# Kernel tuning notes

Measured on AMD Instinct MI355X. Metric: run time of the kernel, lower is better.

## Reference

```python
import jax, jax.numpy as jnp
import numpy as np

SOS_INDEX = 1  # args.sos_index
EOS_INDEX = 2  # args.eos_index

V, H, T, B = 32000, 1024, 32, 64


def setup_inputs() -> dict:
    key = jax.random.key(0)
    ks = jax.random.split(key, 10)
    s = 0.05  # weight scale to keep softmax/tanh in a sane range
    return {
        "E": jax.random.normal(ks[0], (V, H), jnp.float32) * s,          # embedding table
        "W_ih": jax.random.normal(ks[1], (4 * H, H), jnp.float32) * s,   # LSTMCell input weights (i,f,g,o)
        "W_hh": jax.random.normal(ks[2], (4 * H, H), jnp.float32) * s,
        "b_ih": jax.random.normal(ks[3], (4 * H,), jnp.float32) * s,
        "b_hh": jax.random.normal(ks[4], (4 * H,), jnp.float32) * s,
        "W_out": jax.random.normal(ks[5], (V, H), jnp.float32) * s,      # self.out Linear
        "b_out": jnp.zeros((V,), jnp.float32),
        "encoder_hidden": jax.random.normal(ks[6], (B, H), jnp.float32),
        "encoder_cell": jax.random.normal(ks[7], (B, H), jnp.float32),
        "target_var": jax.random.randint(ks[8], (T, B), 0, V),
        "target_max_len": T,
    }


def reference(E, W_ih, W_hh, b_ih, b_hh, W_out, b_out,
              encoder_hidden, encoder_cell, target_var, target_max_len):
    # Eval-mode decode: use_teacher_forcing = False -> greedy argmax feedback.
    batch = encoder_hidden.shape[0]
    x0 = E[jnp.full((batch,), SOS_INDEX)]  # embedding(SOS) for every batch element

    def step(carry, _):
        x, h, c = carry
        # PyTorch LSTMCell: gates ordered (i, f, g, o)
        gates = x @ W_ih.T + b_ih + h @ W_hh.T + b_hh      # [B, 4H]
        i, f, g, o = jnp.split(gates, 4, axis=1)
        c_new = jax.nn.sigmoid(f) * c + jax.nn.sigmoid(i) * jnp.tanh(g)
        h_new = jax.nn.sigmoid(o) * jnp.tanh(c_new)
        logits = h_new @ W_out.T + b_out                    # [B, V]
        mask = jax.nn.softmax(logits, axis=1)[:, EOS_INDEX] # [B]
        # greedy feedback: topk(1) == argmax
        x_next = E[jnp.argmax(logits, axis=1)]              # [B, H]
        return (x_next, h_new, c_new), (logits, mask)

    _, (outputs, masks) = jax.lax.scan(
        step, (x0, encoder_hidden, encoder_cell), None, length=target_max_len)
    return outputs, masks  # [T, B, V], [T, B]
```

## Files before the change

kernel.cpp:

```cpp
#include <hip/hip_runtime.h>
#include <math.h>


typedef short bf16x8 __attribute__((ext_vector_type(8)));
typedef unsigned short ush8 __attribute__((ext_vector_type(8)));
typedef float f32x4 __attribute__((ext_vector_type(4)));

constexpr int kH = 1024;
constexpr int kFH = 4096;
constexpr int kB = 64;
constexpr int kV = 32000;
constexpr int kT = 32;
constexpr int kSOS = 1;
constexpr int kEOS = 2;

__device__ inline unsigned short f2bf(float f) {
  unsigned int u = __float_as_uint(f);
  u += 0x7fffu + ((u >> 16) & 1u);
  return (unsigned short)(u >> 16);
}
__device__ inline float bf2f(unsigned short h) {
  return __uint_as_float(((unsigned int)h) << 16);
}

__global__ __launch_bounds__(256) void init_kernel(
    const float* __restrict__ eh, const float* __restrict__ ec,
    float* __restrict__ ws) {
  int g = blockIdx.x * 256 + threadIdx.x;
  float* h = ws + 65536;
  float* c = ws + 131072;
  if (g < 65536) {
    int u = g >> 6, b = g & 63;
    c[u * 64 + b] = ec[(size_t)b * kH + u];
  } else {
    int i = g - 65536;
    int u = i >> 6, b = i & 63;
    h[i] = eh[(size_t)b * kH + u];
  }
}

__global__ __launch_bounds__(256) void wsplit_kernel(
    const float* __restrict__ W, unsigned short* __restrict__ hi,
    unsigned short* __restrict__ lo) {
  size_t i = ((size_t)blockIdx.x * 256 + threadIdx.x) * 4;
  float4 w = *(const float4*)(W + i);
  unsigned short h0 = f2bf(w.x), h1 = f2bf(w.y), h2 = f2bf(w.z), h3 = f2bf(w.w);
  ushort4 hv = make_ushort4(h0, h1, h2, h3);
  ushort4 lv = make_ushort4(f2bf(w.x - bf2f(h0)), f2bf(w.y - bf2f(h1)),
                            f2bf(w.z - bf2f(h2)), f2bf(w.w - bf2f(h3)));
  *(ushort4*)(hi + i) = hv;
  *(ushort4*)(lo + i) = lv;
}

__global__ __launch_bounds__(256) void gates_kernel(
    const float* __restrict__ Wih, const float* __restrict__ Whh,
    const float* __restrict__ E, const float* __restrict__ h,
    float* __restrict__ part, const float* __restrict__ pmax_g,
    const float* __restrict__ psum_g, const int* __restrict__ pidx_g,
    const float* __restrict__ out_prev, float* __restrict__ mask_prev, int t) {
  __shared__ __align__(16) float Wt[64 * 68];
  __shared__ __align__(16) float Zt[64 * 68];
  __shared__ const float* rowp[64];
  __shared__ float redA[4][64];
  __shared__ int redI[4][64];
  __shared__ float redS[4][64];
  const int tid = threadIdx.x;
  const int s = blockIdx.y;
  const int r0 = blockIdx.x * 64;
  const int phase = s >> 2;
  const int kc0 = (s & 3) * 256;
  const float* __restrict__ W = phase ? Whh : Wih;

  if (!phase) {
    const int b = tid & 63, kq = tid >> 6;
    if (t == 0) {
      if (tid < 64) rowp[tid] = E + (size_t)kSOS * kH;
    } else {
      float mx = -INFINITY;
      int ix = 0x7fffffff;
      for (int k = kq; k < 250; k += 4) {
        float v = pmax_g[k * 64 + b];
        int ii = pidx_g[k * 64 + b];
        if (v > mx || (v == mx && ii < ix)) { mx = v; ix = ii; }
      }
      redA[kq][b] = mx;
      redI[kq][b] = ix;
      __syncthreads();
      if (tid < 64) {
        float M = redA[0][tid];
        int ai = redI[0][tid];
#pragma unroll
        for (int w2 = 1; w2 < 4; ++w2) {
          float v = redA[w2][tid];
          int ii = redI[w2][tid];
          if (v > M || (v == M && ii < ai)) { M = v; ai = ii; }
        }
        rowp[tid] = E + (size_t)ai * kH;
        redA[0][tid] = M;
      }
      if (blockIdx.x == 0) {
        __syncthreads();
        float M = redA[0][b];
        float sacc = 0.f;
        for (int k = kq; k < 250; k += 4)
          sacc += psum_g[k * 64 + b] * expf(pmax_g[k * 64 + b] - M);
        redS[kq][b] = sacc;
        __syncthreads();
        if (tid < 64) {
          float S = redS[0][tid] + redS[1][tid] + redS[2][tid] + redS[3][tid];
          mask_prev[tid] = expf(out_prev[(size_t)tid * kV + kEOS] - M) / S;
        }
      }
    }
  }
  __syncthreads();

  const int tb4 = tid & 15;
  const int tr4 = tid >> 4;
  float acc[4][4];
#pragma unroll
  for (int i = 0; i < 4; ++i)
#pragma unroll
    for (int j = 0; j < 4; ++j) acc[i][j] = 0.f;

  for (int kc = kc0; kc < kc0 + 256; kc += 64) {
#pragma unroll
    for (int l = 0; l < 4; ++l) {
      int f4 = tid + 256 * l;
      int row = f4 >> 4;
      int c4 = f4 & 15;
      float4 w = *(const float4*)(W + (size_t)(r0 + row) * kH + kc + c4 * 4);
      float wv[4] = {w.x, w.y, w.z, w.w};
#pragma unroll
      for (int cc = 0; cc < 4; ++cc) {
        int c = (cc + c4) & 3;
        Wt[(c4 * 4 + c) * 68 + row] = wv[c];
      }
    }
    if (!phase) {
#pragma unroll
      for (int l = 0; l < 4; ++l) {
        int g = tid + 256 * l;
        int zb = g >> 4, k4 = g & 15;
        f32x4 v = *(const f32x4*)(rowp[zb] + kc + k4 * 4);
#pragma unroll
        for (int j = 0; j < 4; ++j) Zt[(k4 * 4 + j) * 68 + zb] = v[j];
      }
    } else {
#pragma unroll
      for (int l = 0; l < 4; ++l) {
        int f4 = tid + 256 * l;
        int kk = f4 >> 4;
        int b4 = f4 & 15;
        *(float4*)(&Zt[kk * 68 + b4 * 4]) =
            *(const float4*)(h + (size_t)(kc + kk) * 64 + b4 * 4);
      }
    }
    __syncthreads();
#pragma unroll
    for (int kk = 0; kk < 64; ++kk) {
      float4 a = *(const float4*)(&Wt[kk * 68 + tr4 * 4]);
      float4 zb = *(const float4*)(&Zt[kk * 68 + tb4 * 4]);
      float av[4] = {a.x, a.y, a.z, a.w};
      float zv[4] = {zb.x, zb.y, zb.z, zb.w};
#pragma unroll
      for (int i = 0; i < 4; ++i)
#pragma unroll
        for (int j = 0; j < 4; ++j) acc[i][j] += av[i] * zv[j];
    }
    __syncthreads();
  }
#pragma unroll
  for (int i = 0; i < 4; ++i) {
    float4 o = make_float4(acc[i][0], acc[i][1], acc[i][2], acc[i][3]);
    *(float4*)(&part[((size_t)s * kFH + r0 + tr4 * 4 + i) * 64 + tb4 * 4]) = o;
  }
}

__global__ __launch_bounds__(256) void lstm_kernel(
    const float* __restrict__ part, const float* __restrict__ bih,
    const float* __restrict__ bhh, float* __restrict__ h,
    float* __restrict__ c, unsigned short* __restrict__ Hhi,
    unsigned short* __restrict__ Hlo) {
  int g = blockIdx.x * 256 + threadIdx.x;
  int b = g & 63, u = g >> 6;
  float gate[4];
#pragma unroll
  for (int ty = 0; ty < 4; ++ty) {
    int r = ty * kH + u;
    float acc = bih[r] + bhh[r];
#pragma unroll
    for (int s2 = 0; s2 < 8; ++s2)
      acc += part[((size_t)s2 * kFH + r) * 64 + b];
    gate[ty] = acc;
  }
  float gi = 1.f / (1.f + expf(-gate[0]));
  float gf = 1.f / (1.f + expf(-gate[1]));
  float gg = tanhf(gate[2]);
  float go = 1.f / (1.f + expf(-gate[3]));
  float cn = gf * c[g] + gi * gg;
  float hn = go * tanhf(cn);
  c[g] = cn;
  h[g] = hn;
  unsigned short hb = f2bf(hn);
  Hhi[(size_t)b * kH + u] = hb;
  Hlo[(size_t)b * kH + u] = f2bf(hn - bf2f(hb));
}

__global__ __launch_bounds__(256) void logits_mfma_kernel(
    const unsigned short* __restrict__ Whi, const unsigned short* __restrict__ Wlo,
    const unsigned short* __restrict__ Hhi, const unsigned short* __restrict__ Hlo,
    const float* __restrict__ bout, float* __restrict__ out,
    float* __restrict__ pmax_g, float* __restrict__ psum_g,
    int* __restrict__ pidx_g) {
  __shared__ __align__(16) unsigned short Hs[8192];
  const int tid = threadIdx.x;
  const int wave = tid >> 6, lane = tid & 63;
  const int m = lane & 15, q = lane >> 4;
  const int v0 = blockIdx.x * 128 + wave * 32;
  const unsigned short* wp0 = Whi + (size_t)(v0 + m) * kH + q * 8;
  const unsigned short* wp1 = Whi + (size_t)(v0 + 16 + m) * kH + q * 8;
  const unsigned short* lp0 = Wlo + (size_t)(v0 + m) * kH + q * 8;
  const unsigned short* lp1 = Wlo + (size_t)(v0 + 16 + m) * kH + q * 8;

  const unsigned short* sptr[4];
  int sdst[4];
#pragma unroll
  for (int l = 0; l < 4; ++l) {
    int g = tid + 256 * l;
    int tile = g >> 9, row = (g >> 3) & 63, cg = g & 7;
    sptr[l] = (tile ? Hlo : Hhi) + (size_t)row * kH + cg * 8;
    sdst[l] = tile * 4096 + row * 64 + ((cg ^ (row & 7)) * 8);
  }

  f32x4 acc[2][4];
#pragma unroll
  for (int tv = 0; tv < 2; ++tv)
#pragma unroll
    for (int bt = 0; bt < 4; ++bt) acc[tv][bt] = (f32x4){0.f, 0.f, 0.f, 0.f};

  struct WF { bf16x8 ah[2], al[2]; };
  WF w0, w1;
  ush8 hreg[4];

  auto loadW = [&](WF& f, int ko) {
    f.ah[0] = *(const bf16x8*)(wp0 + ko);
    f.ah[1] = *(const bf16x8*)(wp1 + ko);
    f.al[0] = *(const bf16x8*)(lp0 + ko);
    f.al[1] = *(const bf16x8*)(lp1 + ko);
  };
  auto loadH = [&](int kc) {
#pragma unroll
    for (int l = 0; l < 4; ++l) hreg[l] = *(const ush8*)(sptr[l] + kc);
  };
  auto readHfrag = [&](bf16x8 bh[4], bf16x8 bl[4], int koff) {
    int gbase = q + (koff >> 3);
#pragma unroll
    for (int bt = 0; bt < 4; ++bt) {
      int row = bt * 16 + m;
      int off = row * 64 + ((gbase ^ (row & 7)) * 8);
      bh[bt] = *(const bf16x8*)(Hs + off);
      bl[bt] = *(const bf16x8*)(Hs + 4096 + off);
    }
  };
  auto mfma3 = [&](const WF& f, bf16x8 bh[4], bf16x8 bl[4]) {
#pragma unroll
    for (int tv = 0; tv < 2; ++tv)
#pragma unroll
      for (int bt = 0; bt < 4; ++bt) {
        acc[tv][bt] = __builtin_amdgcn_mfma_f32_16x16x32_bf16(
            f.ah[tv], bh[bt], acc[tv][bt], 0, 0, 0);
        acc[tv][bt] = __builtin_amdgcn_mfma_f32_16x16x32_bf16(
            f.ah[tv], bl[bt], acc[tv][bt], 0, 0, 0);
        acc[tv][bt] = __builtin_amdgcn_mfma_f32_16x16x32_bf16(
            f.al[tv], bh[bt], acc[tv][bt], 0, 0, 0);
      }
  };

  loadH(0);
  loadW(w0, 0);
  for (int kc = 0; kc < kH; kc += 64) {
    __syncthreads();
#pragma unroll
    for (int l = 0; l < 4; ++l) *(ush8*)(Hs + sdst[l]) = hreg[l];
    __syncthreads();
    if (kc + 64 < kH) loadH(kc + 64);
    bf16x8 bh[4], bl[4];
    loadW(w1, kc + 32);
    readHfrag(bh, bl, 0);
    mfma3(w0, bh, bl);
    if (kc + 64 < kH) loadW(w0, kc + 64);
    readHfrag(bh, bl, 32);
    mfma3(w1, bh, bl);
  }

  float4 bo0 = *(const float4*)(bout + v0 + q * 4);
  float4 bo1 = *(const float4*)(bout + v0 + 16 + q * 4);
#pragma unroll
  for (int tv = 0; tv < 2; ++tv) {
    float4 bo = tv ? bo1 : bo0;
#pragma unroll
    for (int bt = 0; bt < 4; ++bt) {
      int b = bt * 16 + m;
      f32x4 a = acc[tv][bt];
      a[0] += bo.x; a[1] += bo.y; a[2] += bo.z; a[3] += bo.w;
      acc[tv][bt] = a;
      float4 o = make_float4(a[0], a[1], a[2], a[3]);
      *(float4*)(out + (size_t)b * kV + v0 + tv * 16 + q * 4) = o;
    }
  }

  __shared__ float lred[4][4][64];
  __shared__ int lidx[4][4][64];
  __shared__ float bbm[64];
  const int blk = blockIdx.x;
  const int vbase = blk * 128;

#pragma unroll
  for (int bt = 0; bt < 4; ++bt) {
    float pmv = -INFINITY;
    int piv = 0x7fffffff;
#pragma unroll
    for (int tv = 0; tv < 2; ++tv)
#pragma unroll
      for (int r = 0; r < 4; ++r) {
        float val = acc[tv][bt][r];
        int v = vbase + wave * 32 + tv * 16 + q * 4 + r;
        if (val > pmv) { pmv = val; piv = v; }
      }
    lred[wave][q][bt * 16 + m] = pmv;
    lidx[wave][q][bt * 16 + m] = piv;
  }
  __syncthreads();
  if (tid < 64) {
    float bm = -INFINITY;
    int bi = 0x7fffffff;
#pragma unroll
    for (int w = 0; w < 4; ++w)
#pragma unroll
      for (int qq = 0; qq < 4; ++qq) {
        float v2 = lred[w][qq][tid];
        int i2 = lidx[w][qq][tid];
        if (v2 > bm || (v2 == bm && i2 < bi)) { bm = v2; bi = i2; }
      }
    bbm[tid] = bm;
    pmax_g[(size_t)blk * 64 + tid] = bm;
    pidx_g[(size_t)blk * 64 + tid] = bi;
  }
  __syncthreads();
#pragma unroll
  for (int bt = 0; bt < 4; ++bt) {
    float bm = bbm[bt * 16 + m];
    float s = 0.f;
#pragma unroll
    for (int tv = 0; tv < 2; ++tv)
#pragma unroll
      for (int r = 0; r < 4; ++r) s += expf(acc[tv][bt][r] - bm);
    lred[wave][q][bt * 16 + m] = s;
  }
  __syncthreads();
  if (tid < 64) {
    float s = 0.f;
#pragma unroll
    for (int w = 0; w < 4; ++w)
#pragma unroll
      for (int qq = 0; qq < 4; ++qq) s += lred[w][qq][tid];
    psum_g[(size_t)blk * 64 + tid] = s;
  }
}

__global__ __launch_bounds__(256) void final_mask_kernel(
    const float* __restrict__ pm, const float* __restrict__ ps,
    const float* __restrict__ out_t, float* __restrict__ mask) {
  __shared__ float rm[4][64];
  __shared__ float rs[4][64];
  const int tid = threadIdx.x;
  const int b = tid & 63, kq = tid >> 6;
  float mx = -INFINITY;
  for (int k = kq; k < 250; k += 4) {
    float v = pm[k * 64 + b];
    if (v > mx) mx = v;
  }
  rm[kq][b] = mx;
  __syncthreads();
  if (tid < 64) {
    float M = fmaxf(fmaxf(rm[0][tid], rm[1][tid]), fmaxf(rm[2][tid], rm[3][tid]));
    rm[0][tid] = M;
  }
  __syncthreads();
  float M = rm[0][b];
  float s = 0.f;
  for (int k = kq; k < 250; k += 4)
    s += ps[k * 64 + b] * expf(pm[k * 64 + b] - M);
  rs[kq][b] = s;
  __syncthreads();
  if (tid < 64) {
    float S = rs[0][tid] + rs[1][tid] + rs[2][tid] + rs[3][tid];
    mask[tid] = expf(out_t[(size_t)tid * kV + kEOS] - M) / S;
  }
}

extern "C" void kernel_launch(void* const* d_in, const int* in_sizes, int n_in,
                              void* d_out, int out_size, void* d_ws,
                              size_t ws_size, hipStream_t stream) {
  const float* E = (const float*)d_in[0];
  const float* Wih = (const float*)d_in[1];
  const float* Whh = (const float*)d_in[2];
  const float* bih = (const float*)d_in[3];
  const float* bhh = (const float*)d_in[4];
  const float* Wout = (const float*)d_in[5];
  const float* bout = (const float*)d_in[6];
  const float* eh = (const float*)d_in[7];
  const float* ec = (const float*)d_in[8];
  float* out = (float*)d_out;
  float* ws = (float*)d_ws;

  float* h = ws + 65536;
  float* c = ws + 131072;
  float* part = ws + 196608;
  float* pmaxg = ws + 2293760;
  float* psumg = ws + 2310144;
  int* pidxg = (int*)(ws + 2326528);
  unsigned short* Whi = (unsigned short*)(ws + 2359296);
  unsigned short* Wlo = Whi + (size_t)kV * kH;
  unsigned short* Hhi = Wlo + (size_t)kV * kH;
  unsigned short* Hlo = Hhi + (size_t)kB * kH;
  float* maskbase = out + (size_t)kT * kB * kV;

  init_kernel<<<512, 256, 0, stream>>>(eh, ec, ws);
  wsplit_kernel<<<kV, 256, 0, stream>>>(Wout, Whi, Wlo);
  for (int t = 0; t < kT; ++t) {
    float* out_t = out + (size_t)t * kB * kV;
    const float* out_prev = t ? out + (size_t)(t - 1) * kB * kV : nullptr;
    float* mask_prev = t ? maskbase + (size_t)(t - 1) * kB : nullptr;
    gates_kernel<<<dim3(64, 8), 256, 0, stream>>>(
        Wih, Whh, E, h, part, pmaxg, psumg, pidxg, out_prev, mask_prev, t);
    lstm_kernel<<<256, 256, 0, stream>>>(part, bih, bhh, h, c, Hhi, Hlo);
    logits_mfma_kernel<<<250, 256, 0, stream>>>(Whi, Wlo, Hhi, Hlo, bout,
                                                out_t, pmaxg, psumg, pidxg);
  }
  final_mask_kernel<<<1, 256, 0, stream>>>(
      pmaxg, psumg, out + (size_t)(kT - 1) * kB * kV,
      maskbase + (size_t)(kT - 1) * kB);
}
```

Before: 3.390 ms.

## Halve logits tile per block and stream H from global with 3-stage register prefetch

The logits kernel now gives each block 64 vocab rows instead of 128, so it launches 500 blocks instead of 250 and fills more of the GPU's compute units. The shared-memory staging of H and its barriers are removed. Each wave now loads H fragments straight from global memory (mostly L2 hits) through a three-deep register pipeline, fully unrolled over K. The reduction buffers are resized and moved to fit 500 partial results. The cost is redundant H loads per wave and higher register pressure.

```diff
diff --git a/kernel.cpp b/kernel.cpp
--- a/kernel.cpp
+++ b/kernel.cpp
@@ -3,7 +3,6 @@
 
 
 typedef short bf16x8 __attribute__((ext_vector_type(8)));
-typedef unsigned short ush8 __attribute__((ext_vector_type(8)));
 typedef float f32x4 __attribute__((ext_vector_type(4)));
 
 constexpr int kH = 1024;
@@ -13,6 +12,7 @@
 constexpr int kT = 32;
 constexpr int kSOS = 1;
 constexpr int kEOS = 2;
+constexpr int kLB = 500;
 
 __device__ inline unsigned short f2bf(float f) {
   unsigned int u = __float_as_uint(f);
@@ -78,7 +78,7 @@
     } else {
       float mx = -INFINITY;
       int ix = 0x7fffffff;
-      for (int k = kq; k < 250; k += 4) {
+      for (int k = kq; k < kLB; k += 4) {
         float v = pmax_g[k * 64 + b];
         int ii = pidx_g[k * 64 + b];
         if (v > mx || (v == mx && ii < ix)) { mx = v; ix = ii; }
@@ -102,7 +102,7 @@
         __syncthreads();
         float M = redA[0][b];
         float sacc = 0.f;
-        for (int k = kq; k < 250; k += 4)
+        for (int k = kq; k < kLB; k += 4)
           sacc += psum_g[k * 64 + b] * expf(pmax_g[k * 64 + b] - M);
         redS[kq][b] = sacc;
         __syncthreads();
@@ -207,127 +207,89 @@
   Hlo[(size_t)b * kH + u] = f2bf(hn - bf2f(hb));
 }
 
+struct Frag {
+  bf16x8 ah, al, bh[4], bl[4];
+};
+
+__device__ inline void load_frag(Frag& f, const unsigned short* wp,
+                                 const unsigned short* lp,
+                                 const unsigned short* hh,
+                                 const unsigned short* hl, int ko) {
+  f.ah = *(const bf16x8*)(wp + ko);
+  f.al = *(const bf16x8*)(lp + ko);
+#pragma unroll
+  for (int bt = 0; bt < 4; ++bt) {
+    f.bh[bt] = *(const bf16x8*)(hh + bt * 16 * kH + ko);
+    f.bl[bt] = *(const bf16x8*)(hl + bt * 16 * kH + ko);
+  }
+}
+
+__device__ inline void do_mfma(const Frag& f, f32x4 acc[4]) {
+#pragma unroll
+  for (int bt = 0; bt < 4; ++bt) {
+    acc[bt] = __builtin_amdgcn_mfma_f32_16x16x32_bf16(f.ah, f.bh[bt], acc[bt],
+                                                      0, 0, 0);
+    acc[bt] = __builtin_amdgcn_mfma_f32_16x16x32_bf16(f.ah, f.bl[bt], acc[bt],
+                                                      0, 0, 0);
+    acc[bt] = __builtin_amdgcn_mfma_f32_16x16x32_bf16(f.al, f.bh[bt], acc[bt],
+                                                      0, 0, 0);
+  }
+}
+
 __global__ __launch_bounds__(256) void logits_mfma_kernel(
     const unsigned short* __restrict__ Whi, const unsigned short* __restrict__ Wlo,
     const unsigned short* __restrict__ Hhi, const unsigned short* __restrict__ Hlo,
     const float* __restrict__ bout, float* __restrict__ out,
     float* __restrict__ pmax_g, float* __restrict__ psum_g,
     int* __restrict__ pidx_g) {
-  __shared__ __align__(16) unsigned short Hs[8192];
   const int tid = threadIdx.x;
   const int wave = tid >> 6, lane = tid & 63;
   const int m = lane & 15, q = lane >> 4;
-  const int v0 = blockIdx.x * 128 + wave * 32;
-  const unsigned short* wp0 = Whi + (size_t)(v0 + m) * kH + q * 8;
-  const unsigned short* wp1 = Whi + (size_t)(v0 + 16 + m) * kH + q * 8;
-  const unsigned short* lp0 = Wlo + (size_t)(v0 + m) * kH + q * 8;
-  const unsigned short* lp1 = Wlo + (size_t)(v0 + 16 + m) * kH + q * 8;
-
-  const unsigned short* sptr[4];
-  int sdst[4];
-#pragma unroll
-  for (int l = 0; l < 4; ++l) {
-    int g = tid + 256 * l;
-    int tile = g >> 9, row = (g >> 3) & 63, cg = g & 7;
-    sptr[l] = (tile ? Hlo : Hhi) + (size_t)row * kH + cg * 8;
-    sdst[l] = tile * 4096 + row * 64 + ((cg ^ (row & 7)) * 8);
-  }
-
-  f32x4 acc[2][4];
-#pragma unroll
-  for (int tv = 0; tv < 2; ++tv)
-#pragma unroll
-    for (int bt = 0; bt < 4; ++bt) acc[tv][bt] = (f32x4){0.f, 0.f, 0.f, 0.f};
-
-  struct WF { bf16x8 ah[2], al[2]; };
-  WF w0, w1;
-  ush8 hreg[4];
-
-  auto loadW = [&](WF& f, int ko) {
-    f.ah[0] = *(const bf16x8*)(wp0 + ko);
-    f.ah[1] = *(const bf16x8*)(wp1 + ko);
-    f.al[0] = *(const bf16x8*)(lp0 + ko);
-    f.al[1] = *(const bf16x8*)(lp1 + ko);
-  };
-  auto loadH = [&](int kc) {
-#pragma unroll
-    for (int l = 0; l < 4; ++l) hreg[l] = *(const ush8*)(sptr[l] + kc);
-  };
-  auto readHfrag = [&](bf16x8 bh[4], bf16x8 bl[4], int koff) {
-    int gbase = q + (koff >> 3);
-#pragma unroll
-    for (int bt = 0; bt < 4; ++bt) {
-      int row = bt * 16 + m;
-      int off = row * 64 + ((gbase ^ (row & 7)) * 8);
-      bh[bt] = *(const bf16x8*)(Hs + off);
-      bl[bt] = *(const bf16x8*)(Hs + 4096 + off);
-    }
-  };
-  auto mfma3 = [&](const WF& f, bf16x8 bh[4], bf16x8 bl[4]) {
-#pragma unroll
-    for (int tv = 0; tv < 2; ++tv)
-#pragma unroll
-      for (int bt = 0; bt < 4; ++bt) {
-        acc[tv][bt] = __builtin_amdgcn_mfma_f32_16x16x32_bf16(
-            f.ah[tv], bh[bt], acc[tv][bt], 0, 0, 0);
-        acc[tv][bt] = __builtin_amdgcn_mfma_f32_16x16x32_bf16(
-            f.ah[tv], bl[bt], acc[tv][bt], 0, 0, 0);
-        acc[tv][bt] = __builtin_amdgcn_mfma_f32_16x16x32_bf16(
-            f.al[tv], bh[bt], acc[tv][bt], 0, 0, 0);
-      }
-  };
-
-  loadH(0);
-  loadW(w0, 0);
-  for (int kc = 0; kc < kH; kc += 64) {
-    __syncthreads();
-#pragma unroll
-    for (int l = 0; l < 4; ++l) *(ush8*)(Hs + sdst[l]) = hreg[l];
-    __syncthreads();
-    if (kc + 64 < kH) loadH(kc + 64);
-    bf16x8 bh[4], bl[4];
-    loadW(w1, kc + 32);
-    readHfrag(bh, bl, 0);
-    mfma3(w0, bh, bl);
-    if (kc + 64 < kH) loadW(w0, kc + 64);
-    readHfrag(bh, bl, 32);
-    mfma3(w1, bh, bl);
-  }
-
-  float4 bo0 = *(const float4*)(bout + v0 + q * 4);
-  float4 bo1 = *(const float4*)(bout + v0 + 16 + q * 4);
-#pragma unroll
-  for (int tv = 0; tv < 2; ++tv) {
-    float4 bo = tv ? bo1 : bo0;
-#pragma unroll
-    for (int bt = 0; bt < 4; ++bt) {
-      int b = bt * 16 + m;
-      f32x4 a = acc[tv][bt];
-      a[0] += bo.x; a[1] += bo.y; a[2] += bo.z; a[3] += bo.w;
-      acc[tv][bt] = a;
-      float4 o = make_float4(a[0], a[1], a[2], a[3]);
-      *(float4*)(out + (size_t)b * kV + v0 + tv * 16 + q * 4) = o;
-    }
+  const int v0 = blockIdx.x * 64 + wave * 16;
+  const unsigned short* wp = Whi + (size_t)(v0 + m) * kH + q * 8;
+  const unsigned short* lp = Wlo + (size_t)(v0 + m) * kH + q * 8;
+  const unsigned short* hh = Hhi + (size_t)m * kH + q * 8;
+  const unsigned short* hl = Hlo + (size_t)m * kH + q * 8;
+
+  f32x4 acc[4];
+#pragma unroll
+  for (int bt = 0; bt < 4; ++bt) acc[bt] = (f32x4){0.f, 0.f, 0.f, 0.f};
+
+  Frag f[3];
+  load_frag(f[0], wp, lp, hh, hl, 0);
+  load_frag(f[1], wp, lp, hh, hl, 32);
+#pragma unroll
+  for (int i = 0; i < 32; ++i) {
+    if (i + 2 < 32) load_frag(f[(i + 2) % 3], wp, lp, hh, hl, (i + 2) * 32);
+    do_mfma(f[i % 3], acc);
+  }
+
+  float4 bo = *(const float4*)(bout + v0 + q * 4);
+#pragma unroll
+  for (int bt = 0; bt < 4; ++bt) {
+    int b = bt * 16 + m;
+    f32x4 a = acc[bt];
+    a[0] += bo.x; a[1] += bo.y; a[2] += bo.z; a[3] += bo.w;
+    acc[bt] = a;
+    float4 o = make_float4(a[0], a[1], a[2], a[3]);
+    *(float4*)(out + (size_t)b * kV + v0 + q * 4) = o;
   }
 
   __shared__ float lred[4][4][64];
   __shared__ int lidx[4][4][64];
   __shared__ float bbm[64];
   const int blk = blockIdx.x;
-  const int vbase = blk * 128;
 
 #pragma unroll
   for (int bt = 0; bt < 4; ++bt) {
     float pmv = -INFINITY;
     int piv = 0x7fffffff;
 #pragma unroll
-    for (int tv = 0; tv < 2; ++tv)
-#pragma unroll
-      for (int r = 0; r < 4; ++r) {
-        float val = acc[tv][bt][r];
-        int v = vbase + wave * 32 + tv * 16 + q * 4 + r;
-        if (val > pmv) { pmv = val; piv = v; }
-      }
+    for (int r = 0; r < 4; ++r) {
+      float val = acc[bt][r];
+      int v = v0 + q * 4 + r;
+      if (val > pmv) { pmv = val; piv = v; }
+    }
     lred[wave][q][bt * 16 + m] = pmv;
     lidx[wave][q][bt * 16 + m] = piv;
   }
@@ -353,9 +315,7 @@
     float bm = bbm[bt * 16 + m];
     float s = 0.f;
 #pragma unroll
-    for (int tv = 0; tv < 2; ++tv)
-#pragma unroll
-      for (int r = 0; r < 4; ++r) s += expf(acc[tv][bt][r] - bm);
+    for (int r = 0; r < 4; ++r) s += expf(acc[bt][r] - bm);
     lred[wave][q][bt * 16 + m] = s;
   }
   __syncthreads();
@@ -377,7 +337,7 @@
   const int tid = threadIdx.x;
   const int b = tid & 63, kq = tid >> 6;
   float mx = -INFINITY;
-  for (int k = kq; k < 250; k += 4) {
+  for (int k = kq; k < kLB; k += 4) {
     float v = pm[k * 64 + b];
     if (v > mx) mx = v;
   }
@@ -390,7 +350,7 @@
   __syncthreads();
   float M = rm[0][b];
   float s = 0.f;
-  for (int k = kq; k < 250; k += 4)
+  for (int k = kq; k < kLB; k += 4)
     s += ps[k * 64 + b] * expf(pm[k * 64 + b] - M);
   rs[kq][b] = s;
   __syncthreads();
@@ -415,12 +375,12 @@
   float* out = (float*)d_out;
   float* ws = (float*)d_ws;
 
+  float* pmaxg = ws;
+  float* psumg = ws + 32768;
   float* h = ws + 65536;
   float* c = ws + 131072;
   float* part = ws + 196608;
-  float* pmaxg = ws + 2293760;
-  float* psumg = ws + 2310144;
-  int* pidxg = (int*)(ws + 2326528);
+  int* pidxg = (int*)(ws + 2293760);
   unsigned short* Whi = (unsigned short*)(ws + 2359296);
   unsigned short* Wlo = Whi + (size_t)kV * kH;
   unsigned short* Hhi = Wlo + (size_t)kV * kH;
@@ -436,7 +396,7 @@
     gates_kernel<<<dim3(64, 8), 256, 0, stream>>>(
         Wih, Whh, E, h, part, pmaxg, psumg, pidxg, out_prev, mask_prev, t);
     lstm_kernel<<<256, 256, 0, stream>>>(part, bih, bhh, h, c, Hhi, Hlo);
-    logits_mfma_kernel<<<250, 256, 0, stream>>>(Whi, Wlo, Hhi, Hlo, bout,
+    logits_mfma_kernel<<<kLB, 256, 0, stream>>>(Whi, Wlo, Hhi, Hlo, bout,
                                                 out_t, pmaxg, psumg, pidxg);
   }
   final_mask_kernel<<<1, 256, 0, stream>>>(
```

New measurement: 5.665 ms. +67.1%, slower.
